# Kernel tuning notes

Measured on AMD Instinct MI355X. Metric: run time of the kernel, lower is better.

The kernel has to match this reference:

```python
import jax, jax.numpy as jnp
import numpy as np


def setup_inputs() -> dict:
    key = jax.random.key(0)
    k1, k2 = jax.random.split(key)
    b, n, d = 8, 4096, 128
    qk = jax.random.normal(k1, (b, n, d), dtype=jnp.float32)
    v = jax.random.normal(k2, (b, n, d), dtype=jnp.float32)
    return {"qk": qk, "v": v}


def reference(qk, v):
    # qk: [b, n, d] shared query/key tensor; v: [b, n, d]
    b, n, d = qk.shape
    # keys = L2-normalized qk (F.normalize eps=1e-12); queries = raw qk
    k = qk / jnp.maximum(jnp.linalg.norm(qk, axis=-1, keepdims=True), 1e-12)
    scores = jnp.einsum('bie,bje->bij', qk, k) * (d ** -0.5)  # [b, n, n]
    # mask self-attention on the diagonal with -inf
    eye = jnp.eye(n, dtype=bool)
    scores = jnp.where(eye[None, :, :], -jnp.inf, scores)
    attn = jax.nn.softmax(scores, axis=-1)
    out = jnp.einsum('bij,bje->bie', attn, v)  # [b, n, d]
    return out
```

## Files before the change

### kernel.cpp

```cpp
#include <hip/hip_runtime.h>
#include <hip/hip_bf16.h>
#include <stdint.h>

#define BATCH 8
#define SEQN  4096
#define DIM   128
#define NT    32

typedef __attribute__((ext_vector_type(16))) float f32x16;
typedef __bf16 bf16x8 __attribute__((ext_vector_type(8)));

#define GAS __attribute__((address_space(1)))
#define LAS __attribute__((address_space(3)))

__device__ __forceinline__ ushort f2b(float x) {
  union { float f; uint32_t u; } a; a.f = x;
  uint32_t r = a.u + 0x7fffu + ((a.u >> 16) & 1u);
  return (ushort)(r >> 16);
}
__device__ __forceinline__ uint32_t pkbf(float a, float b) {
  union { __bf16 h[2]; uint32_t u; } x;
  x.h[0] = (__bf16)a; x.h[1] = (__bf16)b;
  return x.u;
}


__global__ __launch_bounds__(256) void prep_fused(
    const float* __restrict__ qk, const float* __restrict__ v,
    ushort* __restrict__ qfb, ushort* __restrict__ kfb, ushort* __restrict__ vfb) {
  __shared__ ushort qt_l[32 * 136];
  __shared__ ushort kt_l[32 * 136];
  __shared__ ushort vt_l[32 * 136];
  const int g = blockIdx.x;
  const int t = threadIdx.x;
  const int r = t >> 3, s = t & 7;
  {
    const float* src = qk + (size_t)g * 4096 + r * 128 + s * 16;
    float x[16];
    #pragma unroll
    for (int i = 0; i < 4; ++i) {
      float4 f = ((const float4*)src)[i];
      x[4*i] = f.x; x[4*i+1] = f.y; x[4*i+2] = f.z; x[4*i+3] = f.w;
    }
    float ss = 0.f;
    #pragma unroll
    for (int i = 0; i < 16; ++i) ss += x[i] * x[i];
    ss += __shfl_xor(ss, 1, 64);
    ss += __shfl_xor(ss, 2, 64);
    ss += __shfl_xor(ss, 4, 64);
    float rn = 1.0f / fmaxf(sqrtf(ss), 1e-12f);
    const float SC = 1.44269504088896340736f / 11.313708498984761f;
    float rs = rn * SC;
    #pragma unroll
    for (int j = 0; j < 16; ++j) {
      qt_l[r * 136 + s * 16 + j] = f2b(x[j]);
      kt_l[r * 136 + s * 16 + j] = f2b(x[j] * rs);
    }
  }
  {
    const float* src = v + (size_t)g * 4096 + r * 128 + s * 16;
    #pragma unroll
    for (int i = 0; i < 4; ++i) {
      float4 f = ((const float4*)src)[i];
      vt_l[r * 136 + s * 16 + 4*i]     = f2b(f.x);
      vt_l[r * 136 + s * 16 + 4*i + 1] = f2b(f.y);
      vt_l[r * 136 + s * 16 + 4*i + 2] = f2b(f.z);
      vt_l[r * 136 + s * 16 + 4*i + 3] = f2b(f.w);
    }
  }
  __syncthreads();
  #pragma unroll
  for (int p = 0; p < 2; ++p) {
    int sl = t + 256 * p;
    int qli = sl & 31, grp = sl >> 5;
    union { ushort u[8]; int4 v; } tq, tk, tv;
    #pragma unroll
    for (int j = 0; j < 8; ++j) {
      tq.u[j] = qt_l[qli * 136 + grp * 8 + j];
      tk.u[j] = kt_l[qli * 136 + grp * 8 + j];
    }
    int db = grp >> 2, ks = (grp >> 1) & 1, hh = grp & 1;
    #pragma unroll
    for (int j = 0; j < 8; ++j)
      tv.u[j] = vt_l[(16 * ks + 8 * hh + j) * 136 + 32 * db + qli];
    *(int4*)(qfb + (size_t)g * 4096 + sl * 8) = tq.v;
    *(int4*)(kfb + (size_t)g * 4096 + sl * 8) = tk.v;
    *(int4*)(vfb + (size_t)g * 4096 + sl * 8) = tv.v;
  }
}

__global__ __launch_bounds__(256, 2) void attn_kernel(
    const ushort* __restrict__ qfb, const ushort* __restrict__ kfb,
    const ushort* __restrict__ vfb, float* __restrict__ out) {
  __shared__ ushort lds[40960];

  const int tid = threadIdx.x;
  const int w  = tid >> 6;
  const int l  = tid & 63;
  const int ql = l & 31;
  const int hi = l >> 5;

  const int bidx  = blockIdx.x;
  const int batch = bidx & 7;
  const int qt    = bidx >> 3;
  const int q0    = qt * 64;
  const size_t cb = (size_t)batch * 128;

  const ushort* kq = kfb + (cb + w * 32) * 4096;
  const ushort* vq = vfb + (cb + w * 32) * 4096;
  ushort* myv = lds + w * 8192;
  ushort* ldsq = lds + 32768;

  {
    const ushort* qsrc = qfb + (cb + qt * 2) * 4096 + tid * 8;
    #pragma unroll
    for (int i = 0; i < 4; ++i)
      __builtin_amdgcn_global_load_lds((const GAS uint32_t*)(qsrc + i * 2048),
          (LAS uint32_t*)(ldsq + i * 2048 + tid * 8), 16, 0, 0);
  }

#define STAGE(bsel, t_) do {                                                   \
    const ushort* vsrc_ = vq + (size_t)(t_) * 4096 + l * 8;                    \
    ushort* vdst_ = myv + (bsel) * 4096 + l * 8;                               \
    _Pragma("unroll")                                                          \
    for (int i_ = 0; i_ < 8; ++i_)                                             \
      __builtin_amdgcn_global_load_lds((const GAS uint32_t*)(vsrc_ + i_ * 512),\
          (LAS uint32_t*)(vdst_ + i_ * 512), 16, 0, 0);                        \
  } while (0)

  STAGE(0, 0);
  bf16x8 kf[8];
  {
    const ushort* kt_p = kq + l * 8;
    #pragma unroll
    for (int kc = 0; kc < 8; ++kc) kf[kc] = *(const bf16x8*)(kt_p + kc * 512);
  }
  __syncthreads();

  f32x16 o[8];
  #pragma unroll
  for (int i = 0; i < 8; ++i)
    #pragma unroll
    for (int r = 0; r < 16; ++r) o[i][r] = 0.f;
  float ls0 = 0.f, ls1 = 0.f;

  int buf = 0;
  for (int t = 0; t < NT; ++t) {
    if (t + 1 < NT) STAGE(buf ^ 1, t + 1);
    const bool pfK = (t + 1 < NT);
    const ushort* kp_n = kq + (size_t)(t + 1) * 4096 + l * 8;

    f32x16 st0, st1;
    #pragma unroll
    for (int r = 0; r < 16; ++r) { st0[r] = 0.f; st1[r] = 0.f; }
    const ushort* qlp = ldsq + l * 8;
    #pragma unroll
    for (int kc = 0; kc < 8; ++kc) {
      bf16x8 q0f = *(const bf16x8*)(qlp + kc * 512);
      bf16x8 q1f = *(const bf16x8*)(qlp + 4096 + kc * 512);
      st0 = __builtin_amdgcn_mfma_f32_32x32x16_bf16(kf[kc], q0f, st0, 0, 0, 0);
      st1 = __builtin_amdgcn_mfma_f32_32x32x16_bf16(kf[kc], q1f, st1, 0, 0, 0);
      if (pfK) kf[kc] = *(const bf16x8*)(kp_n + kc * 512);
    }

    const int kvb = w * 1024 + t * 32;
    if (kvb == q0) {
      #pragma unroll
      for (int r = 0; r < 16; ++r) {
        int crow = (r & 3) + 8 * (r >> 2) + 4 * hi;
        if (crow == ql) st0[r] = -1e30f;
      }
    }
    if (kvb == q0 + 32) {
      #pragma unroll
      for (int r = 0; r < 16; ++r) {
        int crow = (r & 3) + 8 * (r >> 2) + 4 * hi;
        if (crow == ql) st1[r] = -1e30f;
      }
    }

    bf16x8 pa0[2];
    {
      float p0[16];
      #pragma unroll
      for (int r = 0; r < 16; ++r) p0[r] = __builtin_amdgcn_exp2f(st0[r]);
      float a = (p0[0] + p0[1]) + (p0[2] + p0[3]);
      float b = (p0[4] + p0[5]) + (p0[6] + p0[7]);
      float c = (p0[8] + p0[9]) + (p0[10] + p0[11]);
      float d = (p0[12] + p0[13]) + (p0[14] + p0[15]);
      ls0 += (a + b) + (c + d);
      uint32_t w0[4][2];
      #pragma unroll
      for (int g4 = 0; g4 < 4; ++g4) {
        w0[g4][0] = pkbf(p0[4 * g4 + 0], p0[4 * g4 + 1]);
        w0[g4][1] = pkbf(p0[4 * g4 + 2], p0[4 * g4 + 3]);
      }
      #pragma unroll
      for (int ks = 0; ks < 2; ++ks) {
        uint32_t a0 = w0[2 * ks][0], b0 = w0[2 * ks + 1][0];
        uint32_t a1 = w0[2 * ks][1], b1 = w0[2 * ks + 1][1];
        asm volatile("v_permlane32_swap_b32 %0, %1" : "+v"(a0), "+v"(b0));
        asm volatile("v_permlane32_swap_b32 %0, %1" : "+v"(a1), "+v"(b1));
        union { uint32_t u[4]; bf16x8 v; } pb;
        pb.u[0] = a0; pb.u[1] = a1; pb.u[2] = b0; pb.u[3] = b1;
        pa0[ks] = pb.v;
      }
    }

    asm volatile("s_waitcnt vmcnt(16)" ::: "memory");

    const ushort* vlp = myv + buf * 4096 + l * 8;
    bf16x8 vv[8];
    #pragma unroll
    for (int i = 0; i < 8; ++i)
      vv[i] = *(const bf16x8*)(vlp + i * 256 * 2);
    #pragma unroll
    for (int db = 0; db < 4; ++db)
      #pragma unroll
      for (int ks = 0; ks < 2; ++ks)
        o[db] = __builtin_amdgcn_mfma_f32_32x32x16_bf16(vv[db * 2 + ks], pa0[ks], o[db], 0, 0, 0);

    bf16x8 pa1[2];
    {
      float p1[16];
      #pragma unroll
      for (int r = 0; r < 16; ++r) p1[r] = __builtin_amdgcn_exp2f(st1[r]);
      float e = (p1[0] + p1[1]) + (p1[2] + p1[3]);
      float f = (p1[4] + p1[5]) + (p1[6] + p1[7]);
      float g = (p1[8] + p1[9]) + (p1[10] + p1[11]);
      float h = (p1[12] + p1[13]) + (p1[14] + p1[15]);
      ls1 += (e + f) + (g + h);
      uint32_t w1[4][2];
      #pragma unroll
      for (int g4 = 0; g4 < 4; ++g4) {
        w1[g4][0] = pkbf(p1[4 * g4 + 0], p1[4 * g4 + 1]);
        w1[g4][1] = pkbf(p1[4 * g4 + 2], p1[4 * g4 + 3]);
      }
      #pragma unroll
      for (int ks = 0; ks < 2; ++ks) {
        uint32_t c0 = w1[2 * ks][0], d0 = w1[2 * ks + 1][0];
        uint32_t c1 = w1[2 * ks][1], d1 = w1[2 * ks + 1][1];
        asm volatile("v_permlane32_swap_b32 %0, %1" : "+v"(c0), "+v"(d0));
        asm volatile("v_permlane32_swap_b32 %0, %1" : "+v"(c1), "+v"(d1));
        union { uint32_t u[4]; bf16x8 v; } pc;
        pc.u[0] = c0; pc.u[1] = c1; pc.u[2] = d0; pc.u[3] = d1;
        pa1[ks] = pc.v;
      }
    }

    #pragma unroll
    for (int db = 0; db < 4; ++db)
      #pragma unroll
      for (int ks = 0; ks < 2; ++ks)
        o[4 + db] = __builtin_amdgcn_mfma_f32_32x32x16_bf16(vv[db * 2 + ks], pa1[ks], o[4 + db], 0, 0, 0);

    buf ^= 1;
  }
#undef STAGE

  __syncthreads();
  float* A  = (float*)lds;
  float* Bb = A + 8448;
  float* lt = A + 16896;
  float* Lf = A + 17408;

  lt[((w * 2 + hi) * 2 + 0) * 32 + ql] = ls0;
  lt[((w * 2 + hi) * 2 + 1) * 32 + ql] = ls1;
  __syncthreads();
  float L0 = 0.f, L1 = 0.f;
  #pragma unroll
  for (int i = 0; i < 8; ++i) {
    L0 += lt[(i * 2 + 0) * 32 + ql];
    L1 += lt[(i * 2 + 1) * 32 + ql];
  }
  if (w == 0 && hi == 0) { Lf[ql] = 1.0f / L0; Lf[32 + ql] = 1.0f / L1; }

  if (w == 3 || w == 1) {
    float* D = (w == 3) ? A : Bb;
    #pragma unroll
    for (int c = 0; c < 2; ++c)
      #pragma unroll
      for (int db = 0; db < 4; ++db)
        #pragma unroll
        for (int g4 = 0; g4 < 4; ++g4)
          *(float4*)(D + (32 * c + ql) * 132 + 32 * db + 8 * g4 + 4 * hi) =
              make_float4(o[c * 4 + db][4 * g4], o[c * 4 + db][4 * g4 + 1],
                          o[c * 4 + db][4 * g4 + 2], o[c * 4 + db][4 * g4 + 3]);
  }
  __syncthreads();
  if (w == 2 || w == 0) {
    float* D = (w == 2) ? A : Bb;
    #pragma unroll
    for (int c = 0; c < 2; ++c)
      #pragma unroll
      for (int db = 0; db < 4; ++db)
        #pragma unroll
        for (int g4 = 0; g4 < 4; ++g4) {
          float* ptr = D + (32 * c + ql) * 132 + 32 * db + 8 * g4 + 4 * hi;
          float4 tv = *(float4*)ptr;
          tv.x += o[c * 4 + db][4 * g4];
          tv.y += o[c * 4 + db][4 * g4 + 1];
          tv.z += o[c * 4 + db][4 * g4 + 2];
          tv.w += o[c * 4 + db][4 * g4 + 3];
          *(float4*)ptr = tv;
        }
  }
  __syncthreads();
  if (w == 0 || w == 2) {
    const int ch = w >> 1;
    float* outb = out + ((size_t)batch * SEQN + q0) * DIM;
    #pragma unroll
    for (int s2 = 0; s2 < 32; ++s2) {
      const int q = 32 * ch + s2;
      const float iv = Lf[q];
      float2 a2 = *(const float2*)(A + q * 132 + 2 * l);
      float2 b2 = *(const float2*)(Bb + q * 132 + 2 * l);
      *(float2*)(outb + (size_t)q * DIM + 2 * l) =
          make_float2((a2.x + b2.x) * iv, (a2.y + b2.y) * iv);
    }
  }
}

extern "C" void kernel_launch(void* const* d_in, const int* in_sizes, int n_in,
                              void* d_out, int out_size, void* d_ws, size_t ws_size,
                              hipStream_t stream) {
  (void)in_sizes; (void)n_in; (void)out_size; (void)ws_size;
  const float* qk = (const float*)d_in[0];
  const float* v  = (const float*)d_in[1];
  float* out = (float*)d_out;
  size_t nelem = (size_t)BATCH * SEQN * DIM;
  ushort* qfb = (ushort*)d_ws;
  ushort* kfb = qfb + nelem;
  ushort* vfb = kfb + nelem;
  prep_fused<<<BATCH * SEQN / 32, 256, 0, stream>>>(qk, v, qfb, kfb, vfb);
  attn_kernel<<<BATCH * (SEQN / 64), 256, 0, stream>>>(qfb, kfb, vfb, out);
}
```

Baseline: 99.64 us.

## Load V straight into registers and shrink LDS for higher occupancy

V tiles are now fetched per wave directly from global memory into registers, prefetched after the PV MFMAs, instead of being double-buffered through LDS with global_load_lds. This drops the LDS footprint from about 80KB to about 53KB and removes the vmcnt wait and the LDS reads of V. The epilogue reduction is split into two halves of the head dimension so it fits in the smaller LDS, and all four waves now share the output stores. The cost is more VGPR pressure from holding vv[8] alongside kf[8] and the accumulators, and the V load latency is exposed within a single iteration.

```diff
diff --git a/kernel.cpp b/kernel.cpp
--- a/kernel.cpp
+++ b/kernel.cpp
@@ -92,7 +92,7 @@
 __global__ __launch_bounds__(256, 2) void attn_kernel(
     const ushort* __restrict__ qfb, const ushort* __restrict__ kfb,
     const ushort* __restrict__ vfb, float* __restrict__ out) {
-  __shared__ ushort lds[40960];
+  __shared__ __align__(16) ushort lds[26752];
 
   const int tid = threadIdx.x;
   const int w  = tid >> 6;
@@ -108,8 +108,7 @@
 
   const ushort* kq = kfb + (cb + w * 32) * 4096;
   const ushort* vq = vfb + (cb + w * 32) * 4096;
-  ushort* myv = lds + w * 8192;
-  ushort* ldsq = lds + 32768;
+  ushort* ldsq = lds;
 
   {
     const ushort* qsrc = qfb + (cb + qt * 2) * 4096 + tid * 8;
@@ -118,22 +117,15 @@
       __builtin_amdgcn_global_load_lds((const GAS uint32_t*)(qsrc + i * 2048),
           (LAS uint32_t*)(ldsq + i * 2048 + tid * 8), 16, 0, 0);
   }
-
-#define STAGE(bsel, t_) do {                                                   \
-    const ushort* vsrc_ = vq + (size_t)(t_) * 4096 + l * 8;                    \
-    ushort* vdst_ = myv + (bsel) * 4096 + l * 8;                               \
-    _Pragma("unroll")                                                          \
-    for (int i_ = 0; i_ < 8; ++i_)                                             \
-      __builtin_amdgcn_global_load_lds((const GAS uint32_t*)(vsrc_ + i_ * 512),\
-          (LAS uint32_t*)(vdst_ + i_ * 512), 16, 0, 0);                        \
-  } while (0)
-
-  STAGE(0, 0);
-  bf16x8 kf[8];
+  bf16x8 kf[8], vv[8];
   {
     const ushort* kt_p = kq + l * 8;
-    #pragma unroll
-    for (int kc = 0; kc < 8; ++kc) kf[kc] = *(const bf16x8*)(kt_p + kc * 512);
+    const ushort* vt_p = vq + l * 8;
+    #pragma unroll
+    for (int i = 0; i < 8; ++i) {
+      kf[i] = *(const bf16x8*)(kt_p + i * 512);
+      vv[i] = *(const bf16x8*)(vt_p + i * 512);
+    }
   }
   __syncthreads();
 
@@ -144,11 +136,10 @@
     for (int r = 0; r < 16; ++r) o[i][r] = 0.f;
   float ls0 = 0.f, ls1 = 0.f;
 
-  int buf = 0;
   for (int t = 0; t < NT; ++t) {
-    if (t + 1 < NT) STAGE(buf ^ 1, t + 1);
-    const bool pfK = (t + 1 < NT);
+    const bool pf = (t + 1 < NT);
     const ushort* kp_n = kq + (size_t)(t + 1) * 4096 + l * 8;
+    const ushort* vp_n = vq + (size_t)(t + 1) * 4096 + l * 8;
 
     f32x16 st0, st1;
     #pragma unroll
@@ -160,7 +151,7 @@
       bf16x8 q1f = *(const bf16x8*)(qlp + 4096 + kc * 512);
       st0 = __builtin_amdgcn_mfma_f32_32x32x16_bf16(kf[kc], q0f, st0, 0, 0, 0);
       st1 = __builtin_amdgcn_mfma_f32_32x32x16_bf16(kf[kc], q1f, st1, 0, 0, 0);
-      if (pfK) kf[kc] = *(const bf16x8*)(kp_n + kc * 512);
+      if (pf) kf[kc] = *(const bf16x8*)(kp_n + kc * 512);
     }
 
     const int kvb = w * 1024 + t * 32;
@@ -207,13 +198,6 @@
       }
     }
 
-    asm volatile("s_waitcnt vmcnt(16)" ::: "memory");
-
-    const ushort* vlp = myv + buf * 4096 + l * 8;
-    bf16x8 vv[8];
-    #pragma unroll
-    for (int i = 0; i < 8; ++i)
-      vv[i] = *(const bf16x8*)(vlp + i * 256 * 2);
     #pragma unroll
     for (int db = 0; db < 4; ++db)
       #pragma unroll
@@ -253,71 +237,75 @@
       #pragma unroll
       for (int ks = 0; ks < 2; ++ks)
         o[4 + db] = __builtin_amdgcn_mfma_f32_32x32x16_bf16(vv[db * 2 + ks], pa1[ks], o[4 + db], 0, 0, 0);
-
-    buf ^= 1;
-  }
-#undef STAGE
+    if (pf) {
+      #pragma unroll
+      for (int i = 0; i < 8; ++i) vv[i] = *(const bf16x8*)(vp_n + i * 512);
+    }
+  }
 
   __syncthreads();
-  float* A  = (float*)lds;
-  float* Bb = A + 8448;
-  float* lt = A + 16896;
-  float* Lf = A + 17408;
+  float* base = (float*)(lds + 8192);
+  float* SA = base;
+  float* SB = base + 4352;
+  float* lt = base + 8704;
+  float* Lf = base + 9216;
 
   lt[((w * 2 + hi) * 2 + 0) * 32 + ql] = ls0;
   lt[((w * 2 + hi) * 2 + 1) * 32 + ql] = ls1;
   __syncthreads();
-  float L0 = 0.f, L1 = 0.f;
+  if (w == 0) {
+    const int c = l >> 5, qq = l & 31;
+    float L = 0.f;
+    #pragma unroll
+    for (int i = 0; i < 8; ++i) L += lt[(i * 2 + c) * 32 + qq];
+    Lf[c * 32 + qq] = 1.0f / L;
+  }
+
+  float* outb = out + ((size_t)batch * SEQN + q0) * DIM;
   #pragma unroll
-  for (int i = 0; i < 8; ++i) {
-    L0 += lt[(i * 2 + 0) * 32 + ql];
-    L1 += lt[(i * 2 + 1) * 32 + ql];
-  }
-  if (w == 0 && hi == 0) { Lf[ql] = 1.0f / L0; Lf[32 + ql] = 1.0f / L1; }
-
-  if (w == 3 || w == 1) {
-    float* D = (w == 3) ? A : Bb;
-    #pragma unroll
-    for (int c = 0; c < 2; ++c)
-      #pragma unroll
-      for (int db = 0; db < 4; ++db)
+  for (int dh = 0; dh < 2; ++dh) {
+    if (w == 1 || w == 3) {
+      float* D = (w == 1) ? SA : SB;
+      #pragma unroll
+      for (int c = 0; c < 2; ++c)
         #pragma unroll
-        for (int g4 = 0; g4 < 4; ++g4)
-          *(float4*)(D + (32 * c + ql) * 132 + 32 * db + 8 * g4 + 4 * hi) =
-              make_float4(o[c * 4 + db][4 * g4], o[c * 4 + db][4 * g4 + 1],
-                          o[c * 4 + db][4 * g4 + 2], o[c * 4 + db][4 * g4 + 3]);
-  }
-  __syncthreads();
-  if (w == 2 || w == 0) {
-    float* D = (w == 2) ? A : Bb;
-    #pragma unroll
-    for (int c = 0; c < 2; ++c)
-      #pragma unroll
-      for (int db = 0; db < 4; ++db)
+        for (int dd = 0; dd < 2; ++dd) {
+          const int db = 2 * dh + dd;
+          #pragma unroll
+          for (int g4 = 0; g4 < 4; ++g4)
+            *(float4*)(D + (32 * c + ql) * 68 + 32 * dd + 8 * g4 + 4 * hi) =
+                make_float4(o[c * 4 + db][4 * g4],     o[c * 4 + db][4 * g4 + 1],
+                            o[c * 4 + db][4 * g4 + 2], o[c * 4 + db][4 * g4 + 3]);
+        }
+    }
+    __syncthreads();
+    if (w == 0 || w == 2) {
+      float* D = (w == 0) ? SA : SB;
+      #pragma unroll
+      for (int c = 0; c < 2; ++c)
         #pragma unroll
-        for (int g4 = 0; g4 < 4; ++g4) {
-          float* ptr = D + (32 * c + ql) * 132 + 32 * db + 8 * g4 + 4 * hi;
-          float4 tv = *(float4*)ptr;
-          tv.x += o[c * 4 + db][4 * g4];
-          tv.y += o[c * 4 + db][4 * g4 + 1];
-          tv.z += o[c * 4 + db][4 * g4 + 2];
-          tv.w += o[c * 4 + db][4 * g4 + 3];
-          *(float4*)ptr = tv;
+        for (int dd = 0; dd < 2; ++dd) {
+          const int db = 2 * dh + dd;
+          #pragma unroll
+          for (int g4 = 0; g4 < 4; ++g4) {
+            float* ptr = D + (32 * c + ql) * 68 + 32 * dd + 8 * g4 + 4 * hi;
+            float4 tv = *(float4*)ptr;
+            tv.x += o[c * 4 + db][4 * g4];
+            tv.y += o[c * 4 + db][4 * g4 + 1];
+            tv.z += o[c * 4 + db][4 * g4 + 2];
+            tv.w += o[c * 4 + db][4 * g4 + 3];
+            *(float4*)ptr = tv;
+          }
         }
-  }
-  __syncthreads();
-  if (w == 0 || w == 2) {
-    const int ch = w >> 1;
-    float* outb = out + ((size_t)batch * SEQN + q0) * DIM;
-    #pragma unroll
-    for (int s2 = 0; s2 < 32; ++s2) {
-      const int q = 32 * ch + s2;
-      const float iv = Lf[q];
-      float2 a2 = *(const float2*)(A + q * 132 + 2 * l);
-      float2 b2 = *(const float2*)(Bb + q * 132 + 2 * l);
-      *(float2*)(outb + (size_t)q * DIM + 2 * l) =
-          make_float2((a2.x + b2.x) * iv, (a2.y + b2.y) * iv);
-    }
+    }
+    __syncthreads();
+    #pragma unroll
+    for (int rr = 0; rr < 16; ++rr) {
+      const int qq = w * 16 + rr;
+      const float val = (SA[qq * 68 + l] + SB[qq * 68 + l]) * Lf[qq];
+      outb[(size_t)qq * DIM + dh * 64 + l] = val;
+    }
+    __syncthreads();
   }
 }
 
```

New measurement: 98.51 us (median of 2 runs). No clear change (-1.1%).
